# Optimization experiments

Hardware: AMD Instinct MI355X
Metric: run time of the kernel (lower is better)

## Reference

```python
import jax, jax.numpy as jnp
import numpy as np
import math

B, T, C = 4, 2048, 2048
NUM_HEADS = 16
HEAD_DIM = C // NUM_HEADS  # 128
ROPE_BASE = 10000.0


def _rope_tables(t, head_dim, dtype):
    # inv_freq over even dims; emb = concat(freqs, freqs)
    inv_freq = 1.0 / (ROPE_BASE ** (jnp.arange(0, head_dim, 2, dtype=jnp.float32) / head_dim))
    pos = jnp.arange(t, dtype=jnp.float32)
    freqs = jnp.einsum('i,j->ij', pos, inv_freq)          # [t, head_dim/2]
    emb = jnp.concatenate([freqs, freqs], axis=-1)        # [t, head_dim]
    return jnp.cos(emb).astype(dtype), jnp.sin(emb).astype(dtype)


def _rotate_half(x):
    x1, x2 = jnp.split(x, 2, axis=-1)
    return jnp.concatenate([-x2, x1], axis=-1)


def setup_inputs() -> dict:
    key = jax.random.key(0)
    ks = jax.random.split(key, 5)
    scale = 1.0 / math.sqrt(C)
    x = jax.random.normal(ks[0], (B, T, C), dtype=jnp.float32)
    wq = jax.random.normal(ks[1], (C, C), dtype=jnp.float32) * scale
    wk = jax.random.normal(ks[2], (C, C), dtype=jnp.float32) * scale
    wv = jax.random.normal(ks[3], (C, C), dtype=jnp.float32) * scale
    wo = jax.random.normal(ks[4], (C, C), dtype=jnp.float32) * scale
    mask = jnp.tril(jnp.ones((T, T), dtype=jnp.int32))[None, None]  # causal [1,1,T,T]
    return {"x": x, "mask": mask, "wq": wq, "wk": wk, "wv": wv, "wo": wo}


def reference(x, mask, wq, wk, wv, wo):
    b, t, c = x.shape
    h, hd = NUM_HEADS, HEAD_DIM
    # torch Linear: y = x @ W.T (W is [out,in])
    q = (x @ wq.T).reshape(b, t, h, hd).transpose(0, 2, 1, 3)  # [b,h,t,hd]
    k = (x @ wk.T).reshape(b, t, h, hd).transpose(0, 2, 1, 3)
    v = (x @ wv.T).reshape(b, t, h, hd).transpose(0, 2, 1, 3)
    cos, sin = _rope_tables(t, hd, x.dtype)  # [t,hd] each, broadcast over b,h
    q = q * cos + _rotate_half(q) * sin
    k = k * cos + _rotate_half(k) * sin
    att = jnp.einsum('bhqd,bhkd->bhqk', q, k) * (1.0 / math.sqrt(hd))
    att = jnp.where(mask == 0, -jnp.inf, att)
    att = jax.nn.softmax(att, axis=-1)
    y = jnp.einsum('bhqk,bhkd->bhqd', att, v)
    y = y.transpose(0, 2, 1, 3).reshape(b, t, c)
    return y @ wo.T
```

## Files before the change

### kernel.cpp

```cpp
#include <hip/hip_runtime.h>
#include <hip/hip_bf16.h>

#define BB 4
#define TT 2048
#define CC 2048
#define NH 16
#define HD 128
#define BT (BB*TT)

using u16 = unsigned short;
typedef __bf16 bf16x8 __attribute__((ext_vector_type(8)));
typedef float  f32x4  __attribute__((ext_vector_type(4)));

#define AS1 __attribute__((address_space(1)))
#define AS3 __attribute__((address_space(3)))

__device__ __forceinline__ float b2f(u16 u){ return __uint_as_float(((unsigned)u) << 16); }
__device__ __forceinline__ u16 f2b(float f){
  unsigned u = __float_as_uint(f);
  u += 0x7FFFu + ((u >> 16) & 1u);
  return (u16)(u >> 16);
}
__device__ __forceinline__ void gld_lds16(const u16* g, u16* l){
  __builtin_amdgcn_global_load_lds((const AS1 void*)g, (AS3 void*)l, 16, 0, 0);
}

__global__ __launch_bounds__(256) void cvt_kernel(const float* __restrict__ in,
                                                  u16* __restrict__ out, int n8)
{
  const int i = blockIdx.x * 256 + threadIdx.x;
  if (i >= n8) return;
  const float4 a = ((const float4*)in)[2*i];
  const float4 b = ((const float4*)in)[2*i + 1];
  uint4 pk;
  pk.x = (unsigned)f2b(a.x) | ((unsigned)f2b(a.y) << 16);
  pk.y = (unsigned)f2b(a.z) | ((unsigned)f2b(a.w) << 16);
  pk.z = (unsigned)f2b(b.x) | ((unsigned)f2b(b.y) << 16);
  pk.w = (unsigned)f2b(b.z) | ((unsigned)f2b(b.w) << 16);
  ((uint4*)out)[i] = pk;
}

template<bool OUT_BF16>
__global__ __launch_bounds__(512, 2) void gemm256(const u16* __restrict__ A,
                                                  const u16* __restrict__ W,
                                                  void* __restrict__ Cv,
                                                  int K, int N)
{
  __shared__ u16 lds[65536];
  const int tid  = threadIdx.x;
  const int lane = tid & 63;
  const int wid  = tid >> 6;
  const int wm   = wid >> 2;
  const int wn   = wid & 3;

  const int nwg  = (int)(gridDim.x * gridDim.y);
  const int orig = (int)(blockIdx.y * gridDim.x + blockIdx.x);
  const int swz  = (orig & 7) * (nwg >> 3) + (orig >> 3);
  const int bx   = swz % (int)gridDim.x;
  const int by   = swz / (int)gridDim.x;
  const long mbase = (long)by * 256;
  const long nbase = (long)bx * 256;

  const int sR  = tid >> 2;
  const int sG8 = (((tid & 3) ^ (sR & 3)) << 3);
  const u16* gA = A + (mbase + sR) * (long)K + sG8;
  const u16* gB = W + (nbase + sR) * (long)K + sG8;
  const long rowK = (long)128 * K;

  const int n   = lane & 15;
  const int g   = lane >> 4;
  const int sl8 = ((g ^ (n & 3)) << 3);
  const int aoff = (wm*128 + n)*32 + sl8;
  const int boff = 8192 + (wn*64 + n)*32 + sl8;

  f32x4 acc[8][4] = {};
  const int NT = K >> 5;

#define STAGE_A(bufi, tt) do { \
    u16* d_ = lds + (bufi)*16384 + tid*8; \
    gld_lds16(gA + (long)(tt)*32,        d_); \
    gld_lds16(gA + rowK + (long)(tt)*32, d_ + 4096); } while(0)
#define STAGE_B(bufi, tt) do { \
    u16* d_ = lds + (bufi)*16384 + 8192 + tid*8; \
    gld_lds16(gB + (long)(tt)*32,        d_); \
    gld_lds16(gB + rowK + (long)(tt)*32, d_ + 4096); } while(0)

  STAGE_A(0, 0); STAGE_B(0, 0);
  STAGE_A(1, 1); STAGE_B(1, 1);
  STAGE_A(2, 2); STAGE_B(2, 2);
  asm volatile("s_waitcnt vmcnt(8)" ::: "memory");
  __builtin_amdgcn_s_barrier();

  for (int t = 0; t < NT; ++t) {
    const u16* Ab = lds + (t & 3) * 16384;
    bf16x8 a0[4], b0[4], a1[4];
    #pragma unroll
    for (int i = 0; i < 4; i++) a0[i] = *(const bf16x8*)&Ab[aoff + i*512];
    #pragma unroll
    for (int j = 0; j < 4; j++) b0[j] = *(const bf16x8*)&Ab[boff + j*512];
    if (t + 3 < NT) STAGE_A((t+3)&3, t+3);
    __builtin_amdgcn_s_barrier();
    __builtin_amdgcn_s_setprio(1);
    #pragma unroll
    for (int i = 0; i < 4; i++)
      #pragma unroll
      for (int j = 0; j < 4; j++)
        acc[i][j] = __builtin_amdgcn_mfma_f32_16x16x32_bf16(a0[i], b0[j], acc[i][j], 0,0,0);
    __builtin_amdgcn_s_setprio(0);
    __builtin_amdgcn_s_barrier();
    #pragma unroll
    for (int i = 0; i < 4; i++) a1[i] = *(const bf16x8*)&Ab[aoff + (i+4)*512];
    if (t + 3 < NT) STAGE_B((t+3)&3, t+3);
    __builtin_amdgcn_s_barrier();
    __builtin_amdgcn_s_setprio(1);
    #pragma unroll
    for (int i = 0; i < 4; i++)
      #pragma unroll
      for (int j = 0; j < 4; j++)
        acc[i+4][j] = __builtin_amdgcn_mfma_f32_16x16x32_bf16(a1[i], b0[j], acc[i+4][j], 0,0,0);
    __builtin_amdgcn_s_setprio(0);
    if (t + 3 < NT)      { asm volatile("s_waitcnt vmcnt(8)" ::: "memory"); }
    else if (t + 2 < NT) { asm volatile("s_waitcnt vmcnt(4)" ::: "memory"); }
    else                 { asm volatile("s_waitcnt vmcnt(0)" ::: "memory"); }
    __builtin_amdgcn_s_barrier();
  }
#undef STAGE_A
#undef STAGE_B

  const int crow0 = g * 4;
  #pragma unroll
  for (int i = 0; i < 8; i++)
    #pragma unroll
    for (int j = 0; j < 4; j++)
      #pragma unroll
      for (int r = 0; r < 4; r++) {
        const long row = mbase + wm*128 + i*16 + crow0 + r;
        const long col = nbase + wn*64  + j*16 + n;
        if (OUT_BF16) ((u16*)Cv)[row*N + col]   = f2b(acc[i][j][r]);
        else          ((float*)Cv)[row*N + col] = acc[i][j][r];
      }
}

__global__ __launch_bounds__(256) void rope_kernel(u16* __restrict__ q, u16* __restrict__ k)
{
  const unsigned idx = blockIdx.x * 256u + threadIdx.x;
  const int d = idx & 63;
  const int h = (idx >> 6) & 15;
  const int t = (idx >> 10) & 2047;
  const int b = idx >> 21;
  const float inv = __expf(-9.210340371976184f * ((float)d * (1.0f/64.0f)));
  const float ang = (float)t * inv;
  float sn, cs;
  sincosf(ang, &sn, &cs);
  const size_t base = ((size_t)(b * TT + t)) * CC + (size_t)h * HD + d;
  const float q0 = b2f(q[base]), q1 = b2f(q[base + 64]);
  q[base]      = f2b(q0*cs - q1*sn);
  q[base + 64] = f2b(q1*cs + q0*sn);
  const float k0 = b2f(k[base]), k1 = b2f(k[base + 64]);
  k[base]      = f2b(k0*cs - k1*sn);
  k[base + 64] = f2b(k1*cs + k0*sn);
}

__global__ __launch_bounds__(256) void transpose_v(const u16* __restrict__ v,
                                                   u16* __restrict__ vt)
{
  __shared__ u16 L[64][136];
  const int tid = threadIdx.x;
  const int t0 = blockIdx.x * 64;
  const int b = blockIdx.y >> 4, h = blockIdx.y & 15;
  #pragma unroll
  for (int it = 0; it < 4; it++) {
    const int row = (tid >> 4) + it*16;
    const int c8 = (tid & 15) * 8;
    *(uint4*)&L[row][c8] = *(const uint4*)(v + ((size_t)(b*TT + t0 + row))*CC + h*HD + c8);
  }
  __syncthreads();
  #pragma unroll
  for (int it = 0; it < 4; it++) {
    const int hd = (tid >> 3) + it*32;
    const int c = (tid & 7) * 8;
    u16 tmp[8];
    #pragma unroll
    for (int j = 0; j < 8; j++) tmp[j] = L[c + j][hd];
    uint4 pk;
    pk.x = (unsigned)tmp[0] | ((unsigned)tmp[1] << 16);
    pk.y = (unsigned)tmp[2] | ((unsigned)tmp[3] << 16);
    pk.z = (unsigned)tmp[4] | ((unsigned)tmp[5] << 16);
    pk.w = (unsigned)tmp[6] | ((unsigned)tmp[7] << 16);
    *(uint4*)(vt + ((size_t)((b*NH + h)*HD + hd))*TT + t0 + c) = pk;
  }
}

#define PS_ST 72
#define OB_ST 136
__global__ __launch_bounds__(256, 2) void attn_mfma(const u16* __restrict__ q,
                                                    const u16* __restrict__ k,
                                                    const u16* __restrict__ vt,
                                                    u16* __restrict__ y)
{
  __shared__ u16 smem[2*64*128 + 128*64 + 4*32*PS_ST];
  u16* Ks = smem;
  u16* Vs = smem + 16384;
  u16* Ps = smem + 16384 + 8192;

  const int tid  = threadIdx.x;
  const int lane = tid & 63;
  const int w    = tid >> 6;
  const int n    = lane & 15;
  const int g    = lane >> 4;
  const int k8   = g * 8;
  const int nx   = n & 7;
  const int qb   = (int)gridDim.x - 1 - (int)blockIdx.x;
  const int bh   = blockIdx.y;
  const int b = bh >> 4, h = bh & 15;

  const u16* Qg  = q  + (size_t)b*TT*CC + (size_t)h*HD;
  const u16* Kg  = k  + (size_t)b*TT*CC + (size_t)h*HD;
  const u16* Vtg = vt + ((size_t)(b*NH + h)*HD) * TT;
  u16*       Yg  = y  + (size_t)b*TT*CC + (size_t)h*HD;

  const int ksrow = tid >> 4;
  const int kgc   = ((tid & 15) ^ (ksrow & 7)) * 8;
  const int vsrow = tid >> 3;
  const int vgc   = ((tid & 7) ^ (vsrow & 7)) * 8;
  const u16* KgS = Kg  + (size_t)ksrow*CC + kgc;
  const u16* VgS = Vtg + (size_t)vsrow*TT + vgc;

  bf16x8 qf[2][4];
  #pragma unroll
  for (int mi = 0; mi < 2; mi++)
    #pragma unroll
    for (int s = 0; s < 4; s++)
      qf[mi][s] = *(const bf16x8*)(Qg + (size_t)(qb*128 + w*32 + mi*16 + n)*CC + s*32 + k8);

  f32x4 o[8][2] = {};
  float lrow[2][4] = {};

  u16* Psw = Ps + w * 32 * PS_ST;
  const float scale = 0.08838834764831845f;
  const int ktmax = 2*qb + 1;

  {
    u16* dk = Ks + tid*8;
    #pragma unroll
    for (int it = 0; it < 4; it++)
      gld_lds16(KgS + (size_t)(it*16)*CC, dk + it*2048);
  }
  __syncthreads();

  for (int kt = 0; kt <= ktmax; kt++) {
    const int p = kt & 1;
    {
      u16* dv = Vs + tid*8;
      #pragma unroll
      for (int it = 0; it < 4; it++)
        gld_lds16(VgS + (size_t)(it*32)*TT + kt*64, dv + it*2048);
    }
    if (kt < ktmax) {
      u16* dk = Ks + (p^1)*8192 + tid*8;
      #pragma unroll
      for (int it = 0; it < 4; it++)
        gld_lds16(KgS + (size_t)((kt+1)*64 + it*16)*CC, dk + it*2048);
    }

    const u16* Kb = Ks + p*8192;
    f32x4 sacc[4][2] = {};
    __builtin_amdgcn_s_setprio(1);
    #pragma unroll
    for (int s = 0; s < 4; s++) {
      #pragma unroll
      for (int j = 0; j < 4; j++) {
        const bf16x8 kb = *(const bf16x8*)&Kb[(16*j + n)*128 + (((s*4 + g) ^ nx) << 3)];
        sacc[j][0] = __builtin_amdgcn_mfma_f32_16x16x32_bf16(qf[0][s], kb, sacc[j][0], 0,0,0);
        sacc[j][1] = __builtin_amdgcn_mfma_f32_16x16x32_bf16(qf[1][s], kb, sacc[j][1], 0,0,0);
      }
    }
    __builtin_amdgcn_s_setprio(0);

    if (kt >= 2*qb) {
      #pragma unroll
      for (int mi = 0; mi < 2; mi++)
        #pragma unroll
        for (int j = 0; j < 4; j++)
          #pragma unroll
          for (int r = 0; r < 4; r++) {
            const int kcol = kt*64 + 16*j + n;
            const int qrow = qb*128 + w*32 + mi*16 + 4*g + r;
            if (kcol > qrow) sacc[j][mi][r] = -1e30f;
          }
    }

    #pragma unroll
    for (int mi = 0; mi < 2; mi++)
      #pragma unroll
      for (int j = 0; j < 4; j++)
        #pragma unroll
        for (int r = 0; r < 4; r++) {
          const float pv = __expf(sacc[j][mi][r] * scale);
          lrow[mi][r] += pv;
          Psw[(mi*16 + 4*g + r)*PS_ST + 16*j + n] = f2b(pv);
        }

    if (kt < ktmax) { asm volatile("s_waitcnt vmcnt(4) lgkmcnt(0)" ::: "memory"); }
    else            { asm volatile("s_waitcnt vmcnt(0) lgkmcnt(0)" ::: "memory"); }
    __builtin_amdgcn_s_barrier();
    asm volatile("" ::: "memory");

    __builtin_amdgcn_s_setprio(1);
    #pragma unroll
    for (int s2 = 0; s2 < 2; s2++) {
      const bf16x8 pa0 = *(const bf16x8*)&Psw[(n)*PS_ST      + s2*32 + k8];
      const bf16x8 pa1 = *(const bf16x8*)&Psw[(16 + n)*PS_ST + s2*32 + k8];
      #pragma unroll
      for (int jo = 0; jo < 8; jo++) {
        const bf16x8 vb = *(const bf16x8*)&Vs[(16*jo + n)*64 + (((s2*4 + g) ^ nx) << 3)];
        o[jo][0] = __builtin_amdgcn_mfma_f32_16x16x32_bf16(pa0, vb, o[jo][0], 0,0,0);
        o[jo][1] = __builtin_amdgcn_mfma_f32_16x16x32_bf16(pa1, vb, o[jo][1], 0,0,0);
      }
    }
    __builtin_amdgcn_s_setprio(0);

    __syncthreads();
  }

  #pragma unroll
  for (int mi = 0; mi < 2; mi++)
    #pragma unroll
    for (int r = 0; r < 4; r++) {
      float sv = lrow[mi][r];
      #pragma unroll
      for (int msk = 1; msk <= 8; msk <<= 1) sv += __shfl_xor(sv, msk);
      lrow[mi][r] = sv;
    }

  u16* Ob = smem;
  #pragma unroll
  for (int mi = 0; mi < 2; mi++) {
    float inv[4];
    #pragma unroll
    for (int r = 0; r < 4; r++) inv[r] = 1.0f / lrow[mi][r];
    #pragma unroll
    for (int jo = 0; jo < 8; jo++)
      #pragma unroll
      for (int r = 0; r < 4; r++)
        Ob[(w*32 + mi*16 + 4*g + r)*OB_ST + 16*jo + n] = f2b(o[jo][mi][r] * inv[r]);
  }
  __syncthreads();
  #pragma unroll
  for (int it = 0; it < 8; it++) {
    const int idx = it*64 + lane;
    const int row = idx >> 4;
    const int ch  = (idx & 15) * 8;
    const uint4 pk = *(const uint4*)&Ob[(w*32 + row)*OB_ST + ch];
    *(uint4*)(Yg + (size_t)(qb*128 + w*32 + row)*CC + ch) = pk;
  }
}

extern "C" void kernel_launch(void* const* d_in, const int* in_sizes, int n_in,
                              void* d_out, int out_size, void* d_ws, size_t ws_size,
                              hipStream_t stream)
{
  const float* x  = (const float*)d_in[0];
  const float* wq = (const float*)d_in[2];
  const float* wk = (const float*)d_in[3];
  const float* wv = (const float*)d_in[4];
  const float* wo = (const float*)d_in[5];

  const size_t NE  = (size_t)BT * CC;
  const size_t NW  = (size_t)CC * CC;
  u16* q  = (u16*)d_ws;
  u16* k  = q  + NE;
  u16* v  = k  + NE;
  u16* y  = v  + NE;
  u16* xb = y  + NE;
  u16* wqb = xb + NE;
  u16* wkb = wqb + NW;
  u16* wvb = wkb + NW;
  u16* wob = wvb + NW;
  u16* vt  = xb;

  cvt_kernel<<<(int)(NE/8/256), 256, 0, stream>>>(x,  xb,  (int)(NE/8));
  cvt_kernel<<<(int)(NW/8/256), 256, 0, stream>>>(wq, wqb, (int)(NW/8));
  cvt_kernel<<<(int)(NW/8/256), 256, 0, stream>>>(wk, wkb, (int)(NW/8));
  cvt_kernel<<<(int)(NW/8/256), 256, 0, stream>>>(wv, wvb, (int)(NW/8));
  cvt_kernel<<<(int)(NW/8/256), 256, 0, stream>>>(wo, wob, (int)(NW/8));

  const dim3 gg(CC/256, BT/256);
  gemm256<true><<<gg, 512, 0, stream>>>(xb, wqb, q, CC, CC);
  gemm256<true><<<gg, 512, 0, stream>>>(xb, wkb, k, CC, CC);
  gemm256<true><<<gg, 512, 0, stream>>>(xb, wvb, v, CC, CC);

  rope_kernel<<<(BB*TT*NH*64)/256, 256, 0, stream>>>(q, k);

  transpose_v<<<dim3(TT/64, BB*NH), 256, 0, stream>>>(v, vt);

  attn_mfma<<<dim3(TT/128, BB*NH), 256, 0, stream>>>(q, k, vt, y);

  gemm256<false><<<gg, 512, 0, stream>>>(y, wob, (float*)d_out, CC, CC);
}
```

Baseline: 640.1 us.

## Software-pipeline LDS fragment loads across k-steps and cut barriers per iteration

```diff
diff --git a/kernel.cpp b/kernel.cpp
--- a/kernel.cpp
+++ b/kernel.cpp
@@ -88,41 +88,76 @@
   STAGE_A(0, 0); STAGE_B(0, 0);
   STAGE_A(1, 1); STAGE_B(1, 1);
   STAGE_A(2, 2); STAGE_B(2, 2);
-  asm volatile("s_waitcnt vmcnt(8)" ::: "memory");
+  asm volatile("s_waitcnt vmcnt(4)" ::: "memory");
   __builtin_amdgcn_s_barrier();
-
-  for (int t = 0; t < NT; ++t) {
-    const u16* Ab = lds + (t & 3) * 16384;
-    bf16x8 a0[4], b0[4], a1[4];
-    #pragma unroll
-    for (int i = 0; i < 4; i++) a0[i] = *(const bf16x8*)&Ab[aoff + i*512];
-    #pragma unroll
-    for (int j = 0; j < 4; j++) b0[j] = *(const bf16x8*)&Ab[boff + j*512];
-    if (t + 3 < NT) STAGE_A((t+3)&3, t+3);
-    __builtin_amdgcn_s_barrier();
-    __builtin_amdgcn_s_setprio(1);
-    #pragma unroll
-    for (int i = 0; i < 4; i++)
-      #pragma unroll
-      for (int j = 0; j < 4; j++)
-        acc[i][j] = __builtin_amdgcn_mfma_f32_16x16x32_bf16(a0[i], b0[j], acc[i][j], 0,0,0);
-    __builtin_amdgcn_s_setprio(0);
-    __builtin_amdgcn_s_barrier();
-    #pragma unroll
-    for (int i = 0; i < 4; i++) a1[i] = *(const bf16x8*)&Ab[aoff + (i+4)*512];
-    if (t + 3 < NT) STAGE_B((t+3)&3, t+3);
-    __builtin_amdgcn_s_barrier();
-    __builtin_amdgcn_s_setprio(1);
-    #pragma unroll
-    for (int i = 0; i < 4; i++)
-      #pragma unroll
-      for (int j = 0; j < 4; j++)
-        acc[i+4][j] = __builtin_amdgcn_mfma_f32_16x16x32_bf16(a1[i], b0[j], acc[i+4][j], 0,0,0);
-    __builtin_amdgcn_s_setprio(0);
-    if (t + 3 < NT)      { asm volatile("s_waitcnt vmcnt(8)" ::: "memory"); }
-    else if (t + 2 < NT) { asm volatile("s_waitcnt vmcnt(4)" ::: "memory"); }
-    else                 { asm volatile("s_waitcnt vmcnt(0)" ::: "memory"); }
-    __builtin_amdgcn_s_barrier();
+  asm volatile("" ::: "memory");
+
+  bf16x8 pa0A[4], pb0A[4], a1A[4], pa0B[4], pb0B[4], a1B[4];
+  #pragma unroll
+  for (int i = 0; i < 4; i++) pa0A[i] = *(const bf16x8*)&lds[aoff + i*512];
+  #pragma unroll
+  for (int j = 0; j < 4; j++) pb0A[j] = *(const bf16x8*)&lds[boff + j*512];
+
+  for (int t = 0; t < NT; t += 2) {
+    {
+      const u16* Ab = lds + (t & 3) * 16384;
+      const u16* Nb = lds + ((t+1) & 3) * 16384;
+      if (t + 3 < NT) STAGE_A((t+3)&3, t+3);
+      #pragma unroll
+      for (int i = 0; i < 4; i++) a1A[i]  = *(const bf16x8*)&Ab[aoff + (i+4)*512];
+      #pragma unroll
+      for (int i = 0; i < 4; i++) pa0B[i] = *(const bf16x8*)&Nb[aoff + i*512];
+      #pragma unroll
+      for (int j = 0; j < 4; j++) pb0B[j] = *(const bf16x8*)&Nb[boff + j*512];
+      if (t + 3 < NT) STAGE_B((t+3)&3, t+3);
+      __builtin_amdgcn_s_setprio(1);
+      #pragma unroll
+      for (int i = 0; i < 4; i++)
+        #pragma unroll
+        for (int j = 0; j < 4; j++)
+          acc[i][j] = __builtin_amdgcn_mfma_f32_16x16x32_bf16(pa0A[i], pb0A[j], acc[i][j], 0,0,0);
+      #pragma unroll
+      for (int i = 0; i < 4; i++)
+        #pragma unroll
+        for (int j = 0; j < 4; j++)
+          acc[i+4][j] = __builtin_amdgcn_mfma_f32_16x16x32_bf16(a1A[i], pb0A[j], acc[i+4][j], 0,0,0);
+      __builtin_amdgcn_s_setprio(0);
+      if (t + 3 < NT) { asm volatile("s_waitcnt vmcnt(4)" ::: "memory"); }
+      else            { asm volatile("s_waitcnt vmcnt(0)" ::: "memory"); }
+      __builtin_amdgcn_s_barrier();
+      asm volatile("" ::: "memory");
+    }
+    {
+      const int u = t + 1;
+      const u16* Ab = lds + (u & 3) * 16384;
+      if (u + 3 < NT) STAGE_A((u+3)&3, u+3);
+      #pragma unroll
+      for (int i = 0; i < 4; i++) a1B[i] = *(const bf16x8*)&Ab[aoff + (i+4)*512];
+      if (u + 1 < NT) {
+        const u16* Nb = lds + ((u+1) & 3) * 16384;
+        #pragma unroll
+        for (int i = 0; i < 4; i++) pa0A[i] = *(const bf16x8*)&Nb[aoff + i*512];
+        #pragma unroll
+        for (int j = 0; j < 4; j++) pb0A[j] = *(const bf16x8*)&Nb[boff + j*512];
+      }
+      if (u + 3 < NT) STAGE_B((u+3)&3, u+3);
+      __builtin_amdgcn_s_setprio(1);
+      #pragma unroll
+      for (int i = 0; i < 4; i++)
+        #pragma unroll
+        for (int j = 0; j < 4; j++)
+          acc[i][j] = __builtin_amdgcn_mfma_f32_16x16x32_bf16(pa0B[i], pb0B[j], acc[i][j], 0,0,0);
+      #pragma unroll
+      for (int i = 0; i < 4; i++)
+        #pragma unroll
+        for (int j = 0; j < 4; j++)
+          acc[i+4][j] = __builtin_amdgcn_mfma_f32_16x16x32_bf16(a1B[i], pb0B[j], acc[i+4][j], 0,0,0);
+      __builtin_amdgcn_s_setprio(0);
+      if (u + 3 < NT) { asm volatile("s_waitcnt vmcnt(4)" ::: "memory"); }
+      else            { asm volatile("s_waitcnt vmcnt(0)" ::: "memory"); }
+      __builtin_amdgcn_s_barrier();
+      asm volatile("" ::: "memory");
+    }
   }
 #undef STAGE_A
 #undef STAGE_B
```

After: 616.9 us. 3.6% less time.
